# Kernel tuning notes

Measured on AMD Instinct MI355X. Metric: run time of the kernel, lower is better.

The kernel has to match this reference:

```python
import jax, jax.numpy as jnp
import numpy as np

B = 16          # number of point clouds in batch
N_COARSE = 1024 # coarse points per cloud (source of features x)
N_FINE = 4096   # fine points per cloud (interpolation targets)
K = 3           # kNN for inverse-distance interpolation
C_IN = 256      # coarse feature channels
C_SKIP = 128    # skip feature channels
H = 512         # MLP hidden width
EPS = 1e-16     # clamp for squared distance (torch_geometric knn_interpolate)
BN_EPS = 1e-5


def setup_inputs() -> dict:
    key = jax.random.key(0)
    ks = jax.random.split(key, 16)
    x = jax.random.normal(ks[0], (B * N_COARSE, C_IN), jnp.float32)
    pos = jax.random.uniform(ks[1], (B * N_COARSE, 3), jnp.float32)
    x_skip = jax.random.normal(ks[2], (B * N_FINE, C_SKIP), jnp.float32)
    pos_skip = jax.random.uniform(ks[3], (B * N_FINE, 3), jnp.float32)
    batch = (jnp.arange(B * N_COARSE) // N_COARSE).astype(jnp.int64)
    batch_skip = (jnp.arange(B * N_FINE) // N_FINE).astype(jnp.int64)
    c0 = C_IN + C_SKIP
    w1 = jax.random.normal(ks[4], (c0, H), jnp.float32) / np.float32(np.sqrt(c0))
    b1 = jax.random.normal(ks[5], (H,), jnp.float32) * 0.01
    g1 = 1.0 + 0.1 * jax.random.normal(ks[6], (H,), jnp.float32)
    be1 = 0.1 * jax.random.normal(ks[7], (H,), jnp.float32)
    m1 = 0.1 * jax.random.normal(ks[8], (H,), jnp.float32)
    v1 = 1.0 + 0.1 * jax.random.uniform(ks[9], (H,), jnp.float32)
    w2 = jax.random.normal(ks[10], (H, H), jnp.float32) / np.float32(np.sqrt(H))
    b2 = jax.random.normal(ks[11], (H,), jnp.float32) * 0.01
    g2 = 1.0 + 0.1 * jax.random.normal(ks[12], (H,), jnp.float32)
    be2 = 0.1 * jax.random.normal(ks[13], (H,), jnp.float32)
    m2 = 0.1 * jax.random.normal(ks[14], (H,), jnp.float32)
    v2 = 1.0 + 0.1 * jax.random.uniform(ks[15], (H,), jnp.float32)
    return {"x": x, "pos": pos, "batch": batch, "x_skip": x_skip,
            "pos_skip": pos_skip, "batch_skip": batch_skip,
            "w1": w1, "b1": b1, "g1": g1, "be1": be1, "m1": m1, "v1": v1,
            "w2": w2, "b2": b2, "g2": g2, "be2": be2, "m2": m2, "v2": v2}


def knn_interpolate(x, pos, pos_skip):
    # Batches are contiguous with equal sizes -> reshape per cloud.
    xb = x.reshape(B, N_COARSE, C_IN)          # [B, n, C]
    pb = pos.reshape(B, N_COARSE, 3)           # [B, n, 3]
    qb = pos_skip.reshape(B, N_FINE, 3)        # [B, m, 3]
    # squared pairwise distances [B, m, n]
    d2 = jnp.sum((qb[:, :, None, :] - pb[:, None, :, :]) ** 2, axis=-1)
    neg_d2k, idx = jax.lax.top_k(-d2, K)       # [B, m, K]
    d2k = -neg_d2k
    w = 1.0 / jnp.maximum(d2k, EPS)            # inverse squared distance
    feats = jax.vmap(lambda xc, ic: xc[ic])(xb, idx)  # [B, m, K, C]
    out = jnp.sum(w[..., None] * feats, axis=2) / jnp.sum(w, axis=2)[..., None]
    return out.reshape(B * N_FINE, C_IN)


def _block(h, w, b, g, be, m, v):
    # Lin -> ReLU -> BatchNorm1d (inference mode, running stats)
    h = jax.nn.relu(h @ w + b)
    return (h - m) * (g / jnp.sqrt(v + BN_EPS)) + be


def reference(x, pos, batch, x_skip, pos_skip, batch_skip,
              w1, b1, g1, be1, m1, v1, w2, b2, g2, be2, m2, v2):
    xi = knn_interpolate(x, pos, pos_skip)       # [M, C_IN]
    h = jnp.concatenate([xi, x_skip], axis=1)    # [M, C_IN + C_SKIP]
    h = _block(h, w1, b1, g1, be1, m1, v1)
    h = _block(h, w2, b2, g2, be2, m2, v2)
    return (h, pos_skip, batch_skip)
```

## Files before the change

### kernel.cpp

```cpp
#include <hip/hip_runtime.h>
#include <hip/hip_bf16.h>
#include <cstddef>
#include <cstdint>

#define NB 16
#define NC 1024
#define NF 4096
#define CIN 256
#define CSKIP 128
#define HW_ 512
#define K1 (CIN + CSKIP)
#define M_ROWS (NB * NF)
#define H_ELEMS ((size_t)M_ROWS * HW_)
#define POS_ELEMS (M_ROWS * 3)

#define QB 64
#define PARTS 4

typedef __attribute__((ext_vector_type(8))) short bf16x8;
typedef __attribute__((ext_vector_type(4))) float f32x4;
typedef __attribute__((ext_vector_type(4))) unsigned int u32x4;

__device__ __forceinline__ unsigned short f2bf(float f) {
    union { __hip_bfloat16 h; unsigned short u; } cv;
    cv.h = __float2bfloat16(f);
    return cv.u;
}
__device__ __forceinline__ float bf2f(unsigned short u) {
    union { __hip_bfloat16 h; unsigned short u; } cv;
    cv.u = u;
    return __bfloat162float(cv.h);
}
__device__ __forceinline__ void split2(float v, unsigned short& hi, unsigned short& lo) {
    hi = f2bf(v);
    lo = f2bf(v - bf2f(hi));
}

#define GLOAD_LDS(gsrc, ldst)                                                            \
    __builtin_amdgcn_global_load_lds((const __attribute__((address_space(1))) void*)(gsrc), \
                                     (__attribute__((address_space(3))) void*)(ldst), 16, 0, 0)

__launch_bounds__(256)
__global__ void knn_interp_kernel(const float* __restrict__ x,
                                  const float* __restrict__ pos,
                                  const float* __restrict__ pos_skip,
                                  unsigned short* __restrict__ Ahi,
                                  unsigned short* __restrict__ Alo)
{
    __shared__ float4 sp4[NC];
    __shared__ float  s_b[QB * PARTS * 3];
    __shared__ int    s_i[QB * PARTS * 3];
    __shared__ int    s_idx[QB * 3];
    __shared__ float  s_w[QB * 3];

    const int tid   = threadIdx.x;
    const int cloud = blockIdx.x >> 6;
    const int chunk = blockIdx.x & 63;

    const float* pbase = pos + (size_t)cloud * NC * 3;
    for (int j = tid; j < NC; j += 256) {
        const float px = pbase[3 * j + 0];
        const float py = pbase[3 * j + 1];
        const float pz = pbase[3 * j + 2];
        sp4[j] = make_float4(px, py, pz, px * px + py * py + pz * pz);
    }
    __syncthreads();

    const int q    = tid & (QB - 1);
    const int part = tid >> 6;
    const float* qp = pos_skip + ((size_t)cloud * NF + chunk * QB + q) * 3;
    const float qx = qp[0], qy = qp[1], qz = qp[2];
    const float ax = -2.f * qx, ay = -2.f * qy, az = -2.f * qz;
    const float qq = qx * qx + qy * qy + qz * qz;

    float b0 = 1e30f, b1 = 1e30f, b2 = 1e30f;
    int   i0 = 0,     i1 = 0,     i2 = 0;
    const int jbase = part * (NC / PARTS);
#pragma unroll 4
    for (int jj = 0; jj < NC / PARTS; ++jj) {
        const int j = jbase + jj;
        const float4 p = sp4[j];
        const float d = fmaf(ax, p.x, fmaf(ay, p.y, fmaf(az, p.z, p.w))) + qq;
        const bool c0 = d < b0, c1 = d < b1, c2 = d < b2;
        const float nb0 = fminf(b0, d);
        const float nb1 = __builtin_amdgcn_fmed3f(b0, b1, d);
        const float nb2 = __builtin_amdgcn_fmed3f(b1, b2, d);
        const int ni0 = c0 ? j : i0;
        const int ni1 = c0 ? i0 : (c1 ? j : i1);
        const int ni2 = c1 ? i1 : (c2 ? j : i2);
        b0 = nb0; b1 = nb1; b2 = nb2;
        i0 = ni0; i1 = ni1; i2 = ni2;
    }
    {
        const int pb = (q * PARTS + part) * 3;
        s_b[pb + 0] = b0; s_b[pb + 1] = b1; s_b[pb + 2] = b2;
        s_i[pb + 0] = i0; s_i[pb + 1] = i1; s_i[pb + 2] = i2;
    }
    __syncthreads();

    if (tid < QB) {
        const int base = tid * PARTS * 3;
        float m0 = s_b[base + 0], m1 = s_b[base + 1], m2 = s_b[base + 2];
        int   a0 = s_i[base + 0], a1 = s_i[base + 1], a2 = s_i[base + 2];
#pragma unroll
        for (int p = 1; p < PARTS; ++p) {
#pragma unroll
            for (int s = 0; s < 3; ++s) {
                const float d = s_b[base + p * 3 + s];
                const int   j = s_i[base + p * 3 + s];
                const bool c0 = d < m0, c1 = d < m1, c2 = d < m2;
                const float n0 = fminf(m0, d);
                const float n1 = __builtin_amdgcn_fmed3f(m0, m1, d);
                const float n2 = __builtin_amdgcn_fmed3f(m1, m2, d);
                const int e0 = c0 ? j : a0;
                const int e1 = c0 ? a0 : (c1 ? j : a1);
                const int e2 = c1 ? a1 : (c2 ? j : a2);
                m0 = n0; m1 = n1; m2 = n2;
                a0 = e0; a1 = e1; a2 = e2;
            }
        }
        const int id[3] = {a0, a1, a2};
        float w[3], tw = 0.f;
#pragma unroll
        for (int s = 0; s < 3; ++s) {
            const float4 p = sp4[id[s]];
            const float dx = qx - p.x, dy = qy - p.y, dz = qz - p.z;
            const float d2 = fmaf(dx, dx, fmaf(dy, dy, dz * dz));
            w[s] = 1.f / fmaxf(d2, 1e-16f);
            tw += w[s];
        }
        const float winv = 1.f / tw;
#pragma unroll
        for (int s = 0; s < 3; ++s) {
            s_idx[tid * 3 + s] = id[s];
            s_w[tid * 3 + s]   = w[s] * winv;
        }
    }
    __syncthreads();

    const int wave = tid >> 6, lane = tid & 63;
    const float* xc = x + (size_t)cloud * NC * CIN;
    const size_t rowbase = (size_t)cloud * NF + chunk * QB;
    for (int qq2 = wave; qq2 < QB; qq2 += 4) {
        const int   j0 = s_idx[qq2 * 3 + 0], j1 = s_idx[qq2 * 3 + 1], j2 = s_idx[qq2 * 3 + 2];
        const float u0 = s_w[qq2 * 3 + 0],   u1 = s_w[qq2 * 3 + 1],   u2 = s_w[qq2 * 3 + 2];
        const float4 f0 = ((const float4*)(xc + (size_t)j0 * CIN))[lane];
        const float4 f1 = ((const float4*)(xc + (size_t)j1 * CIN))[lane];
        const float4 f2 = ((const float4*)(xc + (size_t)j2 * CIN))[lane];
        float o[4];
        o[0] = u0 * f0.x + u1 * f1.x + u2 * f2.x;
        o[1] = u0 * f0.y + u1 * f1.y + u2 * f2.y;
        o[2] = u0 * f0.z + u1 * f1.z + u2 * f2.z;
        o[3] = u0 * f0.w + u1 * f1.w + u2 * f2.w;
        unsigned short h[4], l[4];
#pragma unroll
        for (int c = 0; c < 4; ++c) split2(o[c], h[c], l[c]);
        uint2 hv, lv;
        hv.x = (unsigned)h[0] | ((unsigned)h[1] << 16);
        hv.y = (unsigned)h[2] | ((unsigned)h[3] << 16);
        lv.x = (unsigned)l[0] | ((unsigned)l[1] << 16);
        lv.y = (unsigned)l[2] | ((unsigned)l[3] << 16);
        const size_t ro = (rowbase + qq2) * K1;
        ((uint2*)(Ahi + ro))[lane] = hv;
        ((uint2*)(Alo + ro))[lane] = lv;
    }
}

__launch_bounds__(256)
__global__ void conv_skip_kernel(const float* __restrict__ xs,
                                 unsigned short* __restrict__ Ahi,
                                 unsigned short* __restrict__ Alo)
{
    const int idx = blockIdx.x * 256 + threadIdx.x;
    const int row = idx >> 5;
    const int c4  = idx & 31;
    const float4 v = ((const float4*)(xs + (size_t)row * CSKIP))[c4];
    const float o[4] = {v.x, v.y, v.z, v.w};
    unsigned short h[4], l[4];
#pragma unroll
    for (int c = 0; c < 4; ++c) split2(o[c], h[c], l[c]);
    uint2 hv, lv;
    hv.x = (unsigned)h[0] | ((unsigned)h[1] << 16);
    hv.y = (unsigned)h[2] | ((unsigned)h[3] << 16);
    lv.x = (unsigned)l[0] | ((unsigned)l[1] << 16);
    lv.y = (unsigned)l[2] | ((unsigned)l[3] << 16);
    const size_t off = (size_t)row * K1 + CIN + c4 * 4;
    *(uint2*)(Ahi + off) = hv;
    *(uint2*)(Alo + off) = lv;
}

__launch_bounds__(256)
__global__ void conv_w_kernel(const float* __restrict__ w,
                              unsigned short* __restrict__ WhiT,
                              unsigned short* __restrict__ WloT, int Kd)
{
    const int idx = blockIdx.x * 256 + threadIdx.x;
    if (idx >= Kd * 512) return;
    const int k = idx >> 9;
    const int n = idx & 511;
    const float v = w[(size_t)k * 512 + n];
    unsigned short h, l;
    split2(v, h, l);
    WhiT[(size_t)n * Kd + k] = h;
    WloT[(size_t)n * Kd + k] = l;
}

#define AHI_OFF 0
#define ALO_OFF 16384
#define WHI_OFF 32768
#define WLO_OFF 49152

__device__ __forceinline__ int cswz(int row) {
    return (((row >> 2) & 3) << 2) ^ (((row >> 3) & 1) << 1) ^ ((row >> 4) & 1);
}

template <bool SPLIT_OUT>
__launch_bounds__(256, 2)
__global__ void gemm_bf3s(const unsigned short* __restrict__ Ahi,
                          const unsigned short* __restrict__ Alo,
                          const unsigned short* __restrict__ Whi,
                          const unsigned short* __restrict__ Wlo,
                          int K,
                          const float* __restrict__ bias,
                          const float* __restrict__ gamma,
                          const float* __restrict__ beta,
                          const float* __restrict__ mean,
                          const float* __restrict__ var,
                          float* __restrict__ Cf,
                          unsigned short* __restrict__ Chi,
                          unsigned short* __restrict__ Clo)
{
    __shared__ alignas(16) unsigned char smem[65536];

    const int bid  = blockIdx.x;
    const int xcd  = bid & 7;
    const int slot = bid >> 3;
    const int bx   = slot & 3;
    const int by   = xcd + (slot >> 2) * 8;
    const int bm   = by * 128;
    const int bn   = bx * 128;

    const int tid  = threadIdx.x;
    const int lane = tid & 63;
    const int wv   = tid >> 6;
    const int wr   = wv >> 1;
    const int wc   = wv & 1;

    const int sr  = lane >> 2;
    const int sgp = lane & 3;

    f32x4 acc[4][4];
#pragma unroll
    for (int i = 0; i < 4; ++i)
#pragma unroll
        for (int j = 0; j < 4; ++j) acc[i][j] = (f32x4){0.f, 0.f, 0.f, 0.f};

    auto stage = [&](int buf, int kk) {
#pragma unroll
        for (int i = 0; i < 2; ++i) {
            const int rl = (wv * 2 + i) * 16 + sr;
            const int g  = sgp ^ ((rl >> 1) & 3);
            const unsigned dst = (wv * 2 + i) * 1024 + buf * 8192;
            const size_t roA = (size_t)(bm + rl) * K + kk + g * 8;
            GLOAD_LDS(Ahi + roA, smem + AHI_OFF + dst);
            GLOAD_LDS(Alo + roA, smem + ALO_OFF + dst);
            const size_t roW = (size_t)(bn + rl) * K + kk + g * 8;
            GLOAD_LDS(Whi + roW, smem + WHI_OFF + dst);
            GLOAD_LDS(Wlo + roW, smem + WLO_OFF + dst);
        }
    };

    int cur = 0;
    stage(0, 0);
    const int NT = K / 32;
    for (int t = 0; t < NT; ++t) {
        __syncthreads();
        if (t + 1 < NT) stage(cur ^ 1, (t + 1) * 32);

        const unsigned short* sAh = (const unsigned short*)(smem + AHI_OFF + cur * 8192);
        const unsigned short* sAl = (const unsigned short*)(smem + ALO_OFF + cur * 8192);
        const unsigned short* sWh = (const unsigned short*)(smem + WHI_OFF + cur * 8192);
        const unsigned short* sWl = (const unsigned short*)(smem + WLO_OFF + cur * 8192);

        bf16x8 ah[4], al[4], wh[4], wl[4];
#pragma unroll
        for (int i = 0; i < 4; ++i) {
            const int r  = wr * 64 + i * 16 + (lane & 15);
            const int ga = (lane >> 4) ^ ((r >> 1) & 3);
            ah[i] = *(const bf16x8*)(sAh + r * 32 + ga * 8);
            al[i] = *(const bf16x8*)(sAl + r * 32 + ga * 8);
            const int c  = wc * 64 + i * 16 + (lane & 15);
            const int gb = (lane >> 4) ^ ((c >> 1) & 3);
            wh[i] = *(const bf16x8*)(sWh + c * 32 + gb * 8);
            wl[i] = *(const bf16x8*)(sWl + c * 32 + gb * 8);
        }
#pragma unroll
        for (int i = 0; i < 4; ++i)
#pragma unroll
            for (int j = 0; j < 4; ++j)
                acc[i][j] = __builtin_amdgcn_mfma_f32_16x16x32_bf16(ah[i], wh[j], acc[i][j], 0, 0, 0);
#pragma unroll
        for (int i = 0; i < 4; ++i)
#pragma unroll
            for (int j = 0; j < 4; ++j)
                acc[i][j] = __builtin_amdgcn_mfma_f32_16x16x32_bf16(ah[i], wl[j], acc[i][j], 0, 0, 0);
#pragma unroll
        for (int i = 0; i < 4; ++i)
#pragma unroll
            for (int j = 0; j < 4; ++j)
                acc[i][j] = __builtin_amdgcn_mfma_f32_16x16x32_bf16(al[i], wh[j], acc[i][j], 0, 0, 0);
        cur ^= 1;
    }

    __syncthreads();
    unsigned int* sC = (unsigned int*)smem;

    const int lc  = lane & 15;
    const int lr4 = (lane >> 4) * 4;
#pragma unroll
    for (int j = 0; j < 4; ++j) {
        const int col  = wc * 64 + j * 16 + lc;
        const int colg = bn + col;
        const float s  = gamma[colg] / sqrtf(var[colg] + 1e-5f);
        const float sh = beta[colg] - mean[colg] * s;
        const float bb = bias[colg];
        const int g    = col >> 2;
#pragma unroll
        for (int i = 0; i < 4; ++i) {
            const f32x4 v = acc[i][j];
#pragma unroll
            for (int q = 0; q < 4; ++q) {
                const int row = wr * 64 + i * 16 + lr4 + q;
                const float val = fmaxf(v[q] + bb, 0.f) * s + sh;
                unsigned u;
                if (SPLIT_OUT) {
                    unsigned short h, l;
                    split2(val, h, l);
                    u = (unsigned)h | ((unsigned)l << 16);
                } else {
                    u = __float_as_uint(val);
                }
                sC[row * 128 + ((g ^ cswz(row)) << 2) + (col & 3)] = u;
            }
        }
    }
    __syncthreads();

#pragma unroll
    for (int it = 0; it < 16; ++it) {
        const int row = wv * 32 + it * 2 + (lane >> 5);
        const int g   = lane & 31;
        const u32x4 v = *(const u32x4*)(sC + row * 128 + ((g ^ cswz(row)) << 2));
        const size_t rg = (size_t)(bm + row) * HW_ + bn + g * 4;
        if (SPLIT_OUT) {
            uint2 hv, lv;
            hv.x = (v[0] & 0xffffu) | (v[1] << 16);
            hv.y = (v[2] & 0xffffu) | (v[3] << 16);
            lv.x = (v[0] >> 16) | (v[1] & 0xffff0000u);
            lv.y = (v[2] >> 16) | (v[3] & 0xffff0000u);
            *(uint2*)(Chi + rg) = hv;
            *(uint2*)(Clo + rg) = lv;
        } else {
            *(u32x4*)((unsigned int*)Cf + rg) = v;
        }
    }
}

__launch_bounds__(256)
__global__ void tail_kernel(const float* __restrict__ pos_skip,
                            float* __restrict__ outp, int mode)
{
    const int i = blockIdx.x * 256 + threadIdx.x;
    if (i < POS_ELEMS) outp[i] = pos_skip[i];
    const int bi = i - POS_ELEMS;
    if (bi >= 0 && bi < M_ROWS) {
        if (mode == 0) {
            outp[POS_ELEMS + bi] = (float)(bi >> 12);
        } else {
            ((unsigned long long*)(outp + POS_ELEMS))[bi] = (unsigned long long)(bi >> 12);
        }
    }
}

extern "C" void kernel_launch(void* const* d_in, const int* in_sizes, int n_in,
                              void* d_out, int out_size, void* d_ws, size_t ws_size,
                              hipStream_t stream)
{
    const float* x        = (const float*)d_in[0];
    const float* pos      = (const float*)d_in[1];
    const float* x_skip   = (const float*)d_in[3];
    const float* pos_skip = (const float*)d_in[4];
    const float* w1  = (const float*)d_in[6];
    const float* b1  = (const float*)d_in[7];
    const float* g1  = (const float*)d_in[8];
    const float* be1 = (const float*)d_in[9];
    const float* m1  = (const float*)d_in[10];
    const float* v1  = (const float*)d_in[11];
    const float* w2  = (const float*)d_in[12];
    const float* b2  = (const float*)d_in[13];
    const float* g2  = (const float*)d_in[14];
    const float* be2 = (const float*)d_in[15];
    const float* m2  = (const float*)d_in[16];
    const float* v2  = (const float*)d_in[17];

    float* out = (float*)d_out;

    unsigned short* A1hi = (unsigned short*)d_out;
    unsigned short* A1lo = A1hi + (size_t)M_ROWS * K1;
    unsigned short* W1hi = A1lo + (size_t)M_ROWS * K1;
    unsigned short* W1lo = W1hi + (size_t)512 * K1;
    unsigned short* W2hi = (unsigned short*)(out + H_ELEMS);
    unsigned short* W2lo = W2hi + (size_t)512 * 512;
    unsigned short* h1hi = (unsigned short*)d_ws;
    unsigned short* h1lo = h1hi + H_ELEMS;

    knn_interp_kernel<<<NB * (NF / QB), 256, 0, stream>>>(x, pos, pos_skip, A1hi, A1lo);
    conv_skip_kernel<<<M_ROWS * 32 / 256, 256, 0, stream>>>(x_skip, A1hi, A1lo);
    conv_w_kernel<<<(K1 * 512 + 255) / 256, 256, 0, stream>>>(w1, W1hi, W1lo, K1);
    conv_w_kernel<<<(512 * 512 + 255) / 256, 256, 0, stream>>>(w2, W2hi, W2lo, 512);

    gemm_bf3s<true><<<dim3(4 * (M_ROWS / 128)), 256, 0, stream>>>(
        A1hi, A1lo, W1hi, W1lo, K1, b1, g1, be1, m1, v1,
        nullptr, h1hi, h1lo);

    gemm_bf3s<false><<<dim3(4 * (M_ROWS / 128)), 256, 0, stream>>>(
        h1hi, h1lo, W2hi, W2lo, HW_, b2, g2, be2, m2, v2,
        out, nullptr, nullptr);

    const long long tail = (long long)out_size - (long long)H_ELEMS;
    if (tail > 0) {
        const int mode = (tail - POS_ELEMS >= 2 * M_ROWS) ? 1 : 0;
        tail_kernel<<<(POS_ELEMS + M_ROWS + 255) / 256, 256, 0, stream>>>(
            pos_skip, out + H_ELEMS, mode);
    }
    (void)in_sizes; (void)n_in; (void)ws_size; (void)d_in;
}
```

Measured before the change: 423.9 us.

## Load weight fragments directly from global into registers instead of LDS

The GEMM no longer stages the W hi/lo tiles through shared memory. Each wave reads its B fragments straight from global memory into registers, double-buffered across two register sets, and the k-loop is unrolled by two so the sets can alternate. This cuts LDS traffic and the shared-memory footprint, and may allow more occupancy. The cost is uncoalesced 16-byte global loads that are duplicated across the wr waves, plus higher register pressure.

```diff
diff --git a/kernel.cpp b/kernel.cpp
--- a/kernel.cpp
+++ b/kernel.cpp
@@ -205,11 +205,6 @@
     WloT[(size_t)n * Kd + k] = l;
 }
 
-#define AHI_OFF 0
-#define ALO_OFF 16384
-#define WHI_OFF 32768
-#define WLO_OFF 49152
-
 __device__ __forceinline__ int cswz(int row) {
     return (((row >> 2) & 3) << 2) ^ (((row >> 3) & 1) << 1) ^ ((row >> 4) & 1);
 }
@@ -261,38 +256,32 @@
             const int rl = (wv * 2 + i) * 16 + sr;
             const int g  = sgp ^ ((rl >> 1) & 3);
             const unsigned dst = (wv * 2 + i) * 1024 + buf * 8192;
-            const size_t roA = (size_t)(bm + rl) * K + kk + g * 8;
-            GLOAD_LDS(Ahi + roA, smem + AHI_OFF + dst);
-            GLOAD_LDS(Alo + roA, smem + ALO_OFF + dst);
-            const size_t roW = (size_t)(bn + rl) * K + kk + g * 8;
-            GLOAD_LDS(Whi + roW, smem + WHI_OFF + dst);
-            GLOAD_LDS(Wlo + roW, smem + WLO_OFF + dst);
+            const size_t ro = (size_t)(bm + rl) * K + kk + g * 8;
+            GLOAD_LDS(Ahi + ro, smem + dst);
+            GLOAD_LDS(Alo + ro, smem + 16384 + dst);
         }
     };
 
-    int cur = 0;
-    stage(0, 0);
-    const int NT = K / 32;
-    for (int t = 0; t < NT; ++t) {
-        __syncthreads();
-        if (t + 1 < NT) stage(cur ^ 1, (t + 1) * 32);
-
-        const unsigned short* sAh = (const unsigned short*)(smem + AHI_OFF + cur * 8192);
-        const unsigned short* sAl = (const unsigned short*)(smem + ALO_OFF + cur * 8192);
-        const unsigned short* sWh = (const unsigned short*)(smem + WHI_OFF + cur * 8192);
-        const unsigned short* sWl = (const unsigned short*)(smem + WLO_OFF + cur * 8192);
-
-        bf16x8 ah[4], al[4], wh[4], wl[4];
+    const int klane = (lane >> 4) * 8;
+    auto loadB = [&](int kk, bf16x8* wh, bf16x8* wl) {
+#pragma unroll
+        for (int j = 0; j < 4; ++j) {
+            const size_t c = (size_t)(bn + wc * 64 + j * 16 + (lane & 15));
+            wh[j] = *(const bf16x8*)(Whi + c * K + kk + klane);
+            wl[j] = *(const bf16x8*)(Wlo + c * K + kk + klane);
+        }
+    };
+
+    auto compute = [&](int buf, const bf16x8* wh, const bf16x8* wl) {
+        const unsigned short* sAh = (const unsigned short*)(smem + buf * 8192);
+        const unsigned short* sAl = (const unsigned short*)(smem + 16384 + buf * 8192);
+        bf16x8 ah[4], al[4];
 #pragma unroll
         for (int i = 0; i < 4; ++i) {
             const int r  = wr * 64 + i * 16 + (lane & 15);
             const int ga = (lane >> 4) ^ ((r >> 1) & 3);
             ah[i] = *(const bf16x8*)(sAh + r * 32 + ga * 8);
             al[i] = *(const bf16x8*)(sAl + r * 32 + ga * 8);
-            const int c  = wc * 64 + i * 16 + (lane & 15);
-            const int gb = (lane >> 4) ^ ((c >> 1) & 3);
-            wh[i] = *(const bf16x8*)(sWh + c * 32 + gb * 8);
-            wl[i] = *(const bf16x8*)(sWl + c * 32 + gb * 8);
         }
 #pragma unroll
         for (int i = 0; i < 4; ++i)
@@ -309,7 +298,22 @@
 #pragma unroll
             for (int j = 0; j < 4; ++j)
                 acc[i][j] = __builtin_amdgcn_mfma_f32_16x16x32_bf16(al[i], wh[j], acc[i][j], 0, 0, 0);
-        cur ^= 1;
+    };
+
+    bf16x8 whA[4], wlA[4], whB[4], wlB[4];
+    loadB(0, whA, wlA);
+    stage(0, 0);
+    int buf = 0;
+    const int NT = K / 32;
+    for (int t = 0; t < NT; t += 2) {
+        __syncthreads();
+        if (t + 1 < NT) { stage(buf ^ 1, (t + 1) * 32); loadB((t + 1) * 32, whB, wlB); }
+        compute(buf, whA, wlA);
+        buf ^= 1;
+        __syncthreads();
+        if (t + 2 < NT) { stage(buf ^ 1, (t + 2) * 32); loadB((t + 2) * 32, whA, wlA); }
+        compute(buf, whB, wlB);
+        buf ^= 1;
     }
 
     __syncthreads();
```

Result: slower. 512.8 us (+21.0%).

## Triple-buffer A tiles with explicit vmcnt waits in split-bf16 GEMM

Applied to the files above, without the earlier changes.

Restructures the GEMM main loop so A tiles use a three-deep LDS ring buffer while W tiles stay double-buffered. Prefetch of A runs two k-steps ahead, and each step waits only on the older loads through a partial s_waitcnt vmcnt before a raw barrier, replacing the __syncthreads. The aim is to hide more global-load latency behind the MFMA work. LDS grows from 64KB to 80KB per block, which could limit the two-blocks-per-CU occupancy the launch bounds target. Correctness depends on the vmcnt count matching the number of outstanding loads per stage.

```diff
diff --git a/kernel.cpp b/kernel.cpp
--- a/kernel.cpp
+++ b/kernel.cpp
@@ -205,10 +205,9 @@
     WloT[(size_t)n * Kd + k] = l;
 }
 
-#define AHI_OFF 0
-#define ALO_OFF 16384
-#define WHI_OFF 32768
-#define WLO_OFF 49152
+#define A_BUF_BYTES 16384
+#define W_BASE      49152
+#define SMEM_BYTES  81920
 
 __device__ __forceinline__ int cswz(int row) {
     return (((row >> 2) & 3) << 2) ^ (((row >> 3) & 1) << 1) ^ ((row >> 4) & 1);
@@ -230,7 +229,7 @@
                           unsigned short* __restrict__ Chi,
                           unsigned short* __restrict__ Clo)
 {
-    __shared__ alignas(16) unsigned char smem[65536];
+    __shared__ alignas(16) unsigned char smem[SMEM_BYTES];
 
     const int bid  = blockIdx.x;
     const int xcd  = bid & 7;
@@ -255,33 +254,34 @@
 #pragma unroll
         for (int j = 0; j < 4; ++j) acc[i][j] = (f32x4){0.f, 0.f, 0.f, 0.f};
 
-    auto stage = [&](int buf, int kk) {
+    auto stageA = [&](int ab, int kk) {
 #pragma unroll
         for (int i = 0; i < 2; ++i) {
             const int rl = (wv * 2 + i) * 16 + sr;
             const int g  = sgp ^ ((rl >> 1) & 3);
-            const unsigned dst = (wv * 2 + i) * 1024 + buf * 8192;
-            const size_t roA = (size_t)(bm + rl) * K + kk + g * 8;
-            GLOAD_LDS(Ahi + roA, smem + AHI_OFF + dst);
-            GLOAD_LDS(Alo + roA, smem + ALO_OFF + dst);
-            const size_t roW = (size_t)(bn + rl) * K + kk + g * 8;
-            GLOAD_LDS(Whi + roW, smem + WHI_OFF + dst);
-            GLOAD_LDS(Wlo + roW, smem + WLO_OFF + dst);
+            const unsigned dst = ab * A_BUF_BYTES + (wv * 2 + i) * 1024;
+            const size_t ro = (size_t)(bm + rl) * K + kk + g * 8;
+            GLOAD_LDS(Ahi + ro, smem + dst);
+            GLOAD_LDS(Alo + ro, smem + 8192 + dst);
         }
     };
-
-    int cur = 0;
-    stage(0, 0);
-    const int NT = K / 32;
-    for (int t = 0; t < NT; ++t) {
-        __syncthreads();
-        if (t + 1 < NT) stage(cur ^ 1, (t + 1) * 32);
-
-        const unsigned short* sAh = (const unsigned short*)(smem + AHI_OFF + cur * 8192);
-        const unsigned short* sAl = (const unsigned short*)(smem + ALO_OFF + cur * 8192);
-        const unsigned short* sWh = (const unsigned short*)(smem + WHI_OFF + cur * 8192);
-        const unsigned short* sWl = (const unsigned short*)(smem + WLO_OFF + cur * 8192);
-
+    auto stageW = [&](int wb, int kk) {
+#pragma unroll
+        for (int i = 0; i < 2; ++i) {
+            const int rl = (wv * 2 + i) * 16 + sr;
+            const int g  = sgp ^ ((rl >> 1) & 3);
+            const unsigned dst = W_BASE + wb * A_BUF_BYTES + (wv * 2 + i) * 1024;
+            const size_t ro = (size_t)(bn + rl) * K + kk + g * 8;
+            GLOAD_LDS(Whi + ro, smem + dst);
+            GLOAD_LDS(Wlo + ro, smem + 8192 + dst);
+        }
+    };
+
+    auto compute = [&](int ab, int wb) {
+        const unsigned short* sAh = (const unsigned short*)(smem + ab * A_BUF_BYTES);
+        const unsigned short* sAl = (const unsigned short*)(smem + ab * A_BUF_BYTES + 8192);
+        const unsigned short* sWh = (const unsigned short*)(smem + W_BASE + wb * A_BUF_BYTES);
+        const unsigned short* sWl = (const unsigned short*)(smem + W_BASE + wb * A_BUF_BYTES + 8192);
         bf16x8 ah[4], al[4], wh[4], wl[4];
 #pragma unroll
         for (int i = 0; i < 4; ++i) {
@@ -309,7 +309,26 @@
 #pragma unroll
             for (int j = 0; j < 4; ++j)
                 acc[i][j] = __builtin_amdgcn_mfma_f32_16x16x32_bf16(al[i], wh[j], acc[i][j], 0, 0, 0);
-        cur ^= 1;
+    };
+
+    const int NT = K / 32;
+    stageA(0, 0);
+    stageW(0, 0);
+    stageA(1, 32);
+    int ab = 0;
+    for (int t = 0; t < NT; ++t) {
+        if (t + 1 < NT) asm volatile("s_waitcnt vmcnt(4)" ::: "memory");
+        else            asm volatile("s_waitcnt vmcnt(0)" ::: "memory");
+        __builtin_amdgcn_s_barrier();
+        asm volatile("" ::: "memory");
+        const int wb = t & 1;
+        if (t + 1 < NT) stageW(wb ^ 1, (t + 1) * 32);
+        if (t + 2 < NT) {
+            int a2 = ab + 2; if (a2 >= 3) a2 -= 3;
+            stageA(a2, (t + 2) * 32);
+        }
+        compute(ab, wb);
+        ++ab; if (ab == 3) ab = 0;
     }
 
     __syncthreads();
```

Measured after the change: 414.6 us. 2.2% less time.
